# Kernel tuning notes

Hardware: AMD Instinct MI355X
Metric: run time of the kernel (lower is better)

Reference implementation:

```python
import jax, jax.numpy as jnp
import numpy as np

K = 7            # kernel size per spatial dim
HALF = K // 2    # 3
WIN = K * K      # 49


def _rel_dist():
    # matches torch: meshgrid('ij') of arange(k)-k//2, euclidean dist, flattened row-major
    c = np.arange(K, dtype=np.float32) - HALF
    gi, gj = np.meshgrid(c, c, indexing='ij')
    return jnp.asarray(np.sqrt(gi ** 2 + gj ** 2).reshape(-1))


def _unfold2d(t):
    B, H, W, C = t.shape
    p = jnp.pad(t, ((0, 0), (HALF, HALF), (HALF, HALF), (0, 0)))
    wins = [p[:, i:i + H, j:j + W, :] for i in range(K) for j in range(K)]
    return jnp.stack(wins, axis=3)


def setup_inputs() -> dict:
    key = jax.random.key(0)
    k1, k2, k3, k4, k5 = jax.random.split(key, 5)
    B, H, W, C = 4, 64, 64, 128
    x = jax.random.normal(k1, (B, H, W, C), dtype=jnp.float32)
    W_qkv = jax.random.normal(k2, (C, 3 * C), dtype=jnp.float32) * (C ** -0.5)
    # width_proj is zero-initialized in the module; use small random values to exercise the soft mask
    W_width = jax.random.normal(k3, (C, 1), dtype=jnp.float32) * 0.02
    b_width = jax.random.normal(k4, (1,), dtype=jnp.float32) * 0.02
    W_out = jax.random.normal(k5, (C, C), dtype=jnp.float32) * (C ** -0.5)
    return {"x": x, "W_qkv": W_qkv, "W_width": W_width, "b_width": b_width, "W_out": W_out}


def reference(x, W_qkv, W_width, b_width, W_out):
    B, H, W, C = x.shape
    L = H * W
    scale = C ** -0.5
    rel_dist = _rel_dist()
    max_dist = rel_dist.max()

    qkv = x @ W_qkv                              # (B,H,W,3C)
    q, k, v = jnp.split(qkv, 3, axis=-1)
    width = jax.nn.sigmoid(x @ W_width + b_width) * max_dist + 0.5  # (B,H,W,1)

    k_win = _unfold2d(k).reshape(B, L, WIN, C)
    v_win = _unfold2d(v).reshape(B, L, WIN, C)
    q_flat = q.reshape(B, L, C)
    width_flat = width.reshape(B, L, 1)

    scores = jnp.einsum('blc,blwc->blw', q_flat, k_win) * scale
    soft_mask = jax.nn.sigmoid((width_flat - rel_dist) * 5.0)
    scores = scores - (1.0 - soft_mask) * 10000.0
    attn = jax.nn.softmax(scores, axis=-1)
    out = jnp.einsum('blw,blwc->blc', attn, v_win).reshape(B, H, W, C)
    return (out + v) @ W_out
```

## Files before the change

kernel.cpp:

```cpp
#include <hip/hip_runtime.h>

#define C 128
#define NPIX 16384
#define THREE_C 384

typedef unsigned short u16;
typedef unsigned int u32;
typedef short bf16x8 __attribute__((ext_vector_type(8)));
typedef float f32x4 __attribute__((ext_vector_type(4)));

__device__ __forceinline__ float bf2f(u16 h) { return __uint_as_float(((u32)h) << 16); }
__device__ __forceinline__ u16 f2bf(float f) {
    u32 b = __float_as_uint(f);
    b += 0x7FFF + ((b >> 16) & 1);
    return (u16)(b >> 16);
}
__device__ __forceinline__ u32 pack2(float a, float b) {
    return (u32)f2bf(a) | ((u32)f2bf(b) << 16);
}

#define GST 136

__global__ __launch_bounds__(256) void qkv_kernel(const float* __restrict__ x,
                                                  const float* __restrict__ Wqkv,
                                                  const float* __restrict__ Wwidth,
                                                  const float* __restrict__ bwidth,
                                                  u16* __restrict__ qb,
                                                  u16* __restrict__ kb,
                                                  u16* __restrict__ vb,
                                                  float* __restrict__ width_g) {
    __shared__ u16 xs[64 * GST];
    __shared__ u16 wt[128 * GST];
    const int task = ((int)(blockIdx.x & 7)) * 96 + ((int)blockIdx.x >> 3);
    const int rb = task / 3;
    const int nb = task % 3;
    const int p0 = rb * 64;
    const int tid = threadIdx.x;
    const int wv = tid >> 6;
    const int l = tid & 63;
    const int l15 = l & 15;
    const int l4 = l >> 4;

#pragma unroll
    for (int t = 0; t < 8; ++t) {
        const int f = tid + t * 256;
        const int kq = f & 31, r = f >> 5;
        const float4 xv = *(const float4*)(x + (size_t)(p0 + r) * C + kq * 4);
        uint2 pk;
        pk.x = pack2(xv.x, xv.y);
        pk.y = pack2(xv.z, xv.w);
        *(uint2*)&xs[r * GST + kq * 4] = pk;
    }
#pragma unroll
    for (int t = 0; t < 16; ++t) {
        const int f = tid + t * 256;
        const int c = f & 127, kq = f >> 7;
        const float w0 = Wqkv[(size_t)(kq * 4 + 0) * THREE_C + nb * 128 + c];
        const float w1 = Wqkv[(size_t)(kq * 4 + 1) * THREE_C + nb * 128 + c];
        const float w2 = Wqkv[(size_t)(kq * 4 + 2) * THREE_C + nb * 128 + c];
        const float w3 = Wqkv[(size_t)(kq * 4 + 3) * THREE_C + nb * 128 + c];
        uint2 pk;
        pk.x = pack2(w0, w1);
        pk.y = pack2(w2, w3);
        *(uint2*)&wt[c * GST + kq * 4] = pk;
    }
    __syncthreads();

    if (nb == 0 && tid < 64) {
        float wacc = 0.f;
#pragma unroll
        for (int kk = 0; kk < C; ++kk) wacc += bf2f(xs[tid * GST + kk]) * Wwidth[kk];
        const float z = wacc + bwidth[0];
        width_g[p0 + tid] = (1.f / (1.f + __expf(-z))) * 4.242640687f + 0.5f;
    }

    const int strip = wv * 16;
    bf16x8 af[4];
#pragma unroll
    for (int kf = 0; kf < 4; ++kf)
        af[kf] = *(const bf16x8*)&xs[(strip + l15) * GST + kf * 32 + l4 * 8];

    f32x4 acc[8];
#pragma unroll
    for (int nf = 0; nf < 8; ++nf) acc[nf] = (f32x4){0.f, 0.f, 0.f, 0.f};
#pragma unroll
    for (int nf = 0; nf < 8; ++nf) {
#pragma unroll
        for (int kf = 0; kf < 4; ++kf) {
            const bf16x8 bf = *(const bf16x8*)&wt[(nf * 16 + l15) * GST + kf * 32 + l4 * 8];
            acc[nf] = __builtin_amdgcn_mfma_f32_16x16x32_bf16(af[kf], bf, acc[nf], 0, 0, 0);
        }
    }

    u16* dst = (nb == 0) ? qb : (nb == 1) ? kb : vb;
#pragma unroll
    for (int nf = 0; nf < 8; ++nf) {
        const int col = nf * 16 + l15;
#pragma unroll
        for (int r = 0; r < 4; ++r) {
            const int row = strip + l4 * 4 + r;
            dst[(size_t)(p0 + row) * C + col] = f2bf(acc[nf][r]);
        }
    }
}

#define HSTRIDE 136
#define TSTRIDE 232
#define VSWZ(ch, h) ((h) ^ ((((ch) >> 3) & 3) << 3))

__global__ __launch_bounds__(1024) void attn_kernel(const u16* __restrict__ qb,
                                                    const u16* __restrict__ kb,
                                                    const u16* __restrict__ vb,
                                                    const float* __restrict__ width_g,
                                                    const float* __restrict__ Wout,
                                                    float* __restrict__ out) {
    __shared__ u16 Kl[208 * HSTRIDE];
    __shared__ u16 Vt[128 * TSTRIDE];
    __shared__ u16 Pl[64 * TSTRIDE];
    __shared__ float rmax[4][64];
    __shared__ float rsum[4][64];
    __shared__ float wdl[64];

    const int tid = threadIdx.x;
    const int wv = tid >> 6;
    const int l = tid & 63;
    const int l15 = l & 15;
    const int l4 = l >> 4;

    const int W = ((int)blockIdx.x & 7) * 32 + ((int)blockIdx.x >> 3);
    const int b = W >> 6;
    const int t = W & 63;
    const int i0 = (t >> 3) * 8;
    const int j0 = (t & 7) * 8;
    const int pbase = b * 4096;

    if (tid < 64)
        wdl[tid] = width_g[pbase + (i0 + (tid >> 3)) * 64 + j0 + (tid & 7)];

#pragma unroll
    for (int u = 0; u < 5; ++u) {
        const int f = tid + u * 1024;
        if (f < 3328) {
            const int c = f & 15, h = f >> 4;
            uint4 val = make_uint4(0, 0, 0, 0);
            if (h < 196) {
                const int hi = (h * 2341) >> 15;
                const int hj = h - hi * 14;
                const int ii = i0 - 3 + hi, jj = j0 - 3 + hj;
                if (((unsigned)ii < 64u) && ((unsigned)jj < 64u))
                    val = *(const uint4*)(kb + (size_t)(pbase + ii * 64 + jj) * C + c * 8);
            }
            *(uint4*)&Kl[h * HSTRIDE + c * 8] = val;
        } else {
            const int f2 = f - 3328;
            const int c8 = f2 & 15, h = (f2 >> 4) * 2;
            union { uint4 u4; u16 us[8]; } va, vz;
            va.u4 = make_uint4(0, 0, 0, 0);
            vz.u4 = make_uint4(0, 0, 0, 0);
            {
                const int hi = (h * 2341) >> 15;
                const int hj = h - hi * 14;
                const int ii = i0 - 3 + hi, jj = j0 - 3 + hj;
                if ((h < 196) && ((unsigned)ii < 64u) && ((unsigned)jj < 64u))
                    va.u4 = *(const uint4*)(vb + (size_t)(pbase + ii * 64 + jj) * C + c8 * 8);
            }
            {
                const int h1 = h + 1;
                const int hi = (h1 * 2341) >> 15;
                const int hj = h1 - hi * 14;
                const int ii = i0 - 3 + hi, jj = j0 - 3 + hj;
                if ((h1 < 196) && ((unsigned)ii < 64u) && ((unsigned)jj < 64u))
                    vz.u4 = *(const uint4*)(vb + (size_t)(pbase + ii * 64 + jj) * C + c8 * 8);
            }
#pragma unroll
            for (int s = 0; s < 8; ++s) {
                const int ch = c8 * 8 + s;
                *(u32*)&Vt[ch * TSTRIDE + VSWZ(ch, h)] = (u32)va.us[s] | ((u32)vz.us[s] << 16);
            }
        }
    }

    const int strip = wv >> 2;
    const int g = wv & 3;
    bf16x8 qf[4];
    {
        const int qr = strip * 16 + l15;
        const int p = pbase + (i0 + (qr >> 3)) * 64 + j0 + (qr & 7);
#pragma unroll
        for (int kf = 0; kf < 4; ++kf)
            qf[kf] = *(const bf16x8*)(qb + (size_t)p * C + kf * 32 + l4 * 8);
    }
    __syncthreads();

    f32x4 sv[4];
#pragma unroll
    for (int tt = 0; tt < 4; ++tt) {
        const int nf = g + 4 * tt;
        f32x4 acc = {0.f, 0.f, 0.f, 0.f};
        if (nf < 13) {
            const u16* kr = Kl + (nf * 16 + l15) * HSTRIDE + l4 * 8;
#pragma unroll
            for (int kf = 0; kf < 4; ++kf)
                acc = __builtin_amdgcn_mfma_f32_16x16x32_bf16(
                    qf[kf], *(const bf16x8*)(kr + kf * 32), acc, 0, 0, 0);
        }
        sv[tt] = acc;
    }

    const int qrb = strip * 16 + l4 * 4;
    float wdr[4], mxr[4];
#pragma unroll
    for (int r = 0; r < 4; ++r) { wdr[r] = wdl[qrb + r]; mxr[r] = -3.0e38f; }
#pragma unroll
    for (int tt = 0; tt < 4; ++tt) {
        const int nf = g + 4 * tt;
        if (nf < 13) {
            const int n = nf * 16 + l15;
            const int hi = (n * 2341) >> 15;
            const int hj = n - hi * 14;
#pragma unroll
            for (int r = 0; r < 4; ++r) {
                const int qr = qrb + r;
                const int di = hi - 3 - (qr >> 3);
                const int dj = hj - 3 - (qr & 7);
                const bool valid = ((unsigned)(di + 3) <= 6u) && ((unsigned)(dj + 3) <= 6u);
                float s = -3.0e38f;
                if (valid) {
                    const float rd = sqrtf((float)(di * di + dj * dj));
                    const float sm = 1.f / (1.f + __expf(-5.f * (wdr[r] - rd)));
                    s = sv[tt][r] * 0.08838834765f - (1.f - sm) * 10000.f;
                }
                sv[tt][r] = s;
                mxr[r] = fmaxf(mxr[r], s);
            }
        } else {
#pragma unroll
            for (int r = 0; r < 4; ++r) sv[tt][r] = -3.0e38f;
        }
    }
#pragma unroll
    for (int r = 0; r < 4; ++r) {
        float m = mxr[r];
        m = fmaxf(m, __shfl_xor(m, 1));
        m = fmaxf(m, __shfl_xor(m, 2));
        m = fmaxf(m, __shfl_xor(m, 4));
        m = fmaxf(m, __shfl_xor(m, 8));
        mxr[r] = m;
    }
    float smr[4] = {0.f, 0.f, 0.f, 0.f};
#pragma unroll
    for (int tt = 0; tt < 4; ++tt) {
#pragma unroll
        for (int r = 0; r < 4; ++r) {
            const float e = __expf(sv[tt][r] - mxr[r]);
            sv[tt][r] = e;
            smr[r] += e;
        }
    }
#pragma unroll
    for (int r = 0; r < 4; ++r) {
        float s = smr[r];
        s += __shfl_xor(s, 1);
        s += __shfl_xor(s, 2);
        s += __shfl_xor(s, 4);
        s += __shfl_xor(s, 8);
        smr[r] = s;
    }
    if (l15 == 0) {
#pragma unroll
        for (int r = 0; r < 4; ++r) {
            rmax[g][qrb + r] = mxr[r];
            rsum[g][qrb + r] = smr[r];
        }
    }
    __syncthreads();

    u16* wtl = Kl;
#pragma unroll
    for (int tq = 0; tq < 4; ++tq) {
        const int f = tid + tq * 1024;
        const int c = f & 127, kq = f >> 7;
        const float w0 = Wout[(size_t)(kq * 4 + 0) * C + c];
        const float w1 = Wout[(size_t)(kq * 4 + 1) * C + c];
        const float w2 = Wout[(size_t)(kq * 4 + 2) * C + c];
        const float w3 = Wout[(size_t)(kq * 4 + 3) * C + c];
        uint2 pk;
        pk.x = pack2(w0, w1);
        pk.y = pack2(w2, w3);
        *(uint2*)&wtl[c * GST + kq * 4] = pk;
    }

    float fac[4];
#pragma unroll
    for (int r = 0; r < 4; ++r) {
        const int qr = qrb + r;
        const float m0 = rmax[0][qr], m1 = rmax[1][qr], m2 = rmax[2][qr], m3 = rmax[3][qr];
        const float mf = fmaxf(fmaxf(m0, m1), fmaxf(m2, m3));
        const float tot = rsum[0][qr] * __expf(m0 - mf) + rsum[1][qr] * __expf(m1 - mf)
                        + rsum[2][qr] * __expf(m2 - mf) + rsum[3][qr] * __expf(m3 - mf);
        fac[r] = __expf(mxr[r] - mf) / tot;
    }
#pragma unroll
    for (int tt = 0; tt < 4; ++tt) {
        const int nf = g + 4 * tt;
        if (nf < 13) {
            const int n = nf * 16 + l15;
#pragma unroll
            for (int r = 0; r < 4; ++r)
                Pl[(qrb + r) * TSTRIDE + n] = f2bf(sv[tt][r] * fac[r]);
        } else if (nf == 13) {
            const int n = 208 + l15;
#pragma unroll
            for (int r = 0; r < 4; ++r)
                Pl[(qrb + r) * TSTRIDE + n] = 0;
        }
    }
    __syncthreads();

    f32x4 oacc[2];
    oacc[0] = (f32x4){0.f, 0.f, 0.f, 0.f};
    oacc[1] = (f32x4){0.f, 0.f, 0.f, 0.f};
#pragma unroll
    for (int kf = 0; kf < 7; ++kf) {
        const bf16x8 pa = *(const bf16x8*)(Pl + (strip * 16 + l15) * TSTRIDE + kf * 32 + l4 * 8);
#pragma unroll
        for (int nf2 = 0; nf2 < 2; ++nf2) {
            const int ch = g * 32 + nf2 * 16 + l15;
            const bf16x8 vf = *(const bf16x8*)(Vt + ch * TSTRIDE + VSWZ(ch, kf * 32 + l4 * 8));
            oacc[nf2] = __builtin_amdgcn_mfma_f32_16x16x32_bf16(pa, vf, oacc[nf2], 0, 0, 0);
        }
    }

    u16* ylds = Kl + 128 * GST;
#pragma unroll
    for (int nf2 = 0; nf2 < 2; ++nf2) {
        const int cch = g * 32 + nf2 * 16 + l15;
#pragma unroll
        for (int r = 0; r < 4; ++r) {
            const int qr = qrb + r;
            const int h = 45 + (qr >> 3) * 14 + (qr & 7);
            const float vv = bf2f(Vt[cch * TSTRIDE + VSWZ(cch, h)]);
            ylds[qr * GST + cch] = f2bf(oacc[nf2][r] + vv);
        }
    }
    __syncthreads();

    bf16x8 yf[4];
#pragma unroll
    for (int kf = 0; kf < 4; ++kf)
        yf[kf] = *(const bf16x8*)&ylds[(strip * 16 + l15) * GST + kf * 32 + l4 * 8];

    f32x4 oc[2];
    oc[0] = (f32x4){0.f, 0.f, 0.f, 0.f};
    oc[1] = (f32x4){0.f, 0.f, 0.f, 0.f};
#pragma unroll
    for (int u = 0; u < 2; ++u) {
        const int nf = g + 4 * u;
#pragma unroll
        for (int kf = 0; kf < 4; ++kf) {
            const bf16x8 bf = *(const bf16x8*)&wtl[(nf * 16 + l15) * GST + kf * 32 + l4 * 8];
            oc[u] = __builtin_amdgcn_mfma_f32_16x16x32_bf16(yf[kf], bf, oc[u], 0, 0, 0);
        }
    }
#pragma unroll
    for (int u = 0; u < 2; ++u) {
        const int col = (g + 4 * u) * 16 + l15;
#pragma unroll
        for (int r = 0; r < 4; ++r) {
            const int qr = qrb + r;
            const int p = pbase + (i0 + (qr >> 3)) * 64 + j0 + (qr & 7);
            out[(size_t)p * C + col] = oc[u][r];
        }
    }
}

extern "C" void kernel_launch(void* const* d_in, const int* in_sizes, int n_in,
                              void* d_out, int out_size, void* d_ws, size_t ws_size,
                              hipStream_t stream) {
    const float* x      = (const float*)d_in[0];
    const float* Wqkv   = (const float*)d_in[1];
    const float* Wwidth = (const float*)d_in[2];
    const float* bwidth = (const float*)d_in[3];
    const float* Wout   = (const float*)d_in[4];
    float* out = (float*)d_out;

    u16* qb = (u16*)d_ws;
    u16* kb = qb + (size_t)NPIX * C;
    u16* vb = kb + (size_t)NPIX * C;
    float* width = (float*)(vb + (size_t)NPIX * C);

    qkv_kernel<<<768, 256, 0, stream>>>(x, Wqkv, Wwidth, bwidth, qb, kb, vb, width);
    attn_kernel<<<256, 1024, 0, stream>>>(qb, kb, vb, width, Wout, out);
}
```

Before: 30.01 us.

## Pretranspose Wout to bf16 in qkv kernel and batch K/V halo loads

The first kernel now converts W_out once into a transposed bf16 buffer in the workspace. The attention kernel prefetches that buffer into registers early and writes it to LDS later, replacing 256 blocks each doing strided fp32 loads and packing. The K/V halo gather is restructured so all global loads are issued before any LDS stores, which raises memory-level parallelism at the cost of more registers. The Vt row stride is also padded slightly to change the LDS bank mapping.

```diff
diff --git a/kernel.cpp b/kernel.cpp
--- a/kernel.cpp
+++ b/kernel.cpp
@@ -25,10 +25,12 @@
                                                   const float* __restrict__ Wqkv,
                                                   const float* __restrict__ Wwidth,
                                                   const float* __restrict__ bwidth,
+                                                  const float* __restrict__ Wout,
                                                   u16* __restrict__ qb,
                                                   u16* __restrict__ kb,
                                                   u16* __restrict__ vb,
-                                                  float* __restrict__ width_g) {
+                                                  float* __restrict__ width_g,
+                                                  u16* __restrict__ wot) {
     __shared__ u16 xs[64 * GST];
     __shared__ u16 wt[128 * GST];
     const int task = ((int)(blockIdx.x & 7)) * 96 + ((int)blockIdx.x >> 3);
@@ -64,6 +66,16 @@
         pk.y = pack2(w2, w3);
         *(uint2*)&wt[c * GST + kq * 4] = pk;
     }
+    if (task < 8) {
+        const int base = (task * 256 + tid) * 8;
+        const int c = base >> 7, k0 = base & 127;
+        uint4 pk;
+        pk.x = pack2(Wout[(size_t)(k0 + 0) * C + c], Wout[(size_t)(k0 + 1) * C + c]);
+        pk.y = pack2(Wout[(size_t)(k0 + 2) * C + c], Wout[(size_t)(k0 + 3) * C + c]);
+        pk.z = pack2(Wout[(size_t)(k0 + 4) * C + c], Wout[(size_t)(k0 + 5) * C + c]);
+        pk.w = pack2(Wout[(size_t)(k0 + 6) * C + c], Wout[(size_t)(k0 + 7) * C + c]);
+        *(uint4*)&wot[base] = pk;
+    }
     __syncthreads();
 
     if (nb == 0 && tid < 64) {
@@ -105,14 +117,14 @@
 }
 
 #define HSTRIDE 136
-#define TSTRIDE 232
+#define TSTRIDE 236
 #define VSWZ(ch, h) ((h) ^ ((((ch) >> 3) & 3) << 3))
 
 __global__ __launch_bounds__(1024) void attn_kernel(const u16* __restrict__ qb,
                                                     const u16* __restrict__ kb,
                                                     const u16* __restrict__ vb,
                                                     const float* __restrict__ width_g,
-                                                    const float* __restrict__ Wout,
+                                                    const u16* __restrict__ wot,
                                                     float* __restrict__ out) {
     __shared__ u16 Kl[208 * HSTRIDE];
     __shared__ u16 Vt[128 * TSTRIDE];
@@ -137,32 +149,42 @@
     if (tid < 64)
         wdl[tid] = width_g[pbase + (i0 + (tid >> 3)) * 64 + j0 + (tid & 7)];
 
-#pragma unroll
-    for (int u = 0; u < 5; ++u) {
-        const int f = tid + u * 1024;
-        if (f < 3328) {
-            const int c = f & 15, h = f >> 4;
-            uint4 val = make_uint4(0, 0, 0, 0);
-            if (h < 196) {
-                const int hi = (h * 2341) >> 15;
-                const int hj = h - hi * 14;
-                const int ii = i0 - 3 + hi, jj = j0 - 3 + hj;
-                if (((unsigned)ii < 64u) && ((unsigned)jj < 64u))
-                    val = *(const uint4*)(kb + (size_t)(pbase + ii * 64 + jj) * C + c * 8);
-            }
-            *(uint4*)&Kl[h * HSTRIDE + c * 8] = val;
-        } else {
-            const int f2 = f - 3328;
-            const int c8 = f2 & 15, h = (f2 >> 4) * 2;
-            union { uint4 u4; u16 us[8]; } va, vz;
-            va.u4 = make_uint4(0, 0, 0, 0);
-            vz.u4 = make_uint4(0, 0, 0, 0);
+    const uint4 z4 = make_uint4(0, 0, 0, 0);
+    uint4 kreg[4];
+    int koff[4];
+    bool kw[4];
+#pragma unroll
+    for (int rr = 0; rr < 4; ++rr) {
+        const int f = tid + rr * 1024;
+        kw[rr] = (f < 3328);
+        kreg[rr] = z4;
+        const int c = f & 15, h = f >> 4;
+        koff[rr] = h * HSTRIDE + c * 8;
+        if (kw[rr] && h < 196) {
+            const int hi = (h * 2341) >> 15;
+            const int hj = h - hi * 14;
+            const int ii = i0 - 3 + hi, jj = j0 - 3 + hj;
+            if (((unsigned)ii < 64u) && ((unsigned)jj < 64u))
+                kreg[rr] = *(const uint4*)(kb + (size_t)(pbase + ii * 64 + jj) * C + c * 8);
+        }
+    }
+    uint4 va[2], vz[2];
+    int vc8[2], vh[2];
+    bool vw[2];
+#pragma unroll
+    for (int rr = 0; rr < 2; ++rr) {
+        const int f = tid + rr * 1024;
+        vw[rr] = (f < 1792);
+        va[rr] = z4; vz[rr] = z4;
+        const int c8 = f & 15, h = ((f >> 4) * 2) & 255;
+        vc8[rr] = c8; vh[rr] = h;
+        if (vw[rr]) {
             {
                 const int hi = (h * 2341) >> 15;
                 const int hj = h - hi * 14;
                 const int ii = i0 - 3 + hi, jj = j0 - 3 + hj;
                 if ((h < 196) && ((unsigned)ii < 64u) && ((unsigned)jj < 64u))
-                    va.u4 = *(const uint4*)(vb + (size_t)(pbase + ii * 64 + jj) * C + c8 * 8);
+                    va[rr] = *(const uint4*)(vb + (size_t)(pbase + ii * 64 + jj) * C + c8 * 8);
             }
             {
                 const int h1 = h + 1;
@@ -170,12 +192,23 @@
                 const int hj = h1 - hi * 14;
                 const int ii = i0 - 3 + hi, jj = j0 - 3 + hj;
                 if ((h1 < 196) && ((unsigned)ii < 64u) && ((unsigned)jj < 64u))
-                    vz.u4 = *(const uint4*)(vb + (size_t)(pbase + ii * 64 + jj) * C + c8 * 8);
+                    vz[rr] = *(const uint4*)(vb + (size_t)(pbase + ii * 64 + jj) * C + c8 * 8);
             }
+        }
+    }
+#pragma unroll
+    for (int rr = 0; rr < 4; ++rr)
+        if (kw[rr]) *(uint4*)&Kl[koff[rr]] = kreg[rr];
+#pragma unroll
+    for (int rr = 0; rr < 2; ++rr) {
+        if (vw[rr]) {
+            union { uint4 u4; u16 us[8]; } ua, uz;
+            ua.u4 = va[rr]; uz.u4 = vz[rr];
+            const int c8 = vc8[rr], h = vh[rr];
 #pragma unroll
             for (int s = 0; s < 8; ++s) {
                 const int ch = c8 * 8 + s;
-                *(u32*)&Vt[ch * TSTRIDE + VSWZ(ch, h)] = (u32)va.us[s] | ((u32)vz.us[s] << 16);
+                *(u32*)&Vt[ch * TSTRIDE + VSWZ(ch, h)] = (u32)ua.us[s] | ((u32)uz.us[s] << 16);
             }
         }
     }
@@ -206,6 +239,9 @@
         }
         sv[tt] = acc;
     }
+
+    uint4 wcopy0 = *(const uint4*)(wot + tid * 8);
+    uint4 wcopy1 = *(const uint4*)(wot + (tid + 1024) * 8);
 
     const int qrb = strip * 16 + l4 * 4;
     float wdr[4], mxr[4];
@@ -276,18 +312,11 @@
     __syncthreads();
 
     u16* wtl = Kl;
-#pragma unroll
-    for (int tq = 0; tq < 4; ++tq) {
-        const int f = tid + tq * 1024;
-        const int c = f & 127, kq = f >> 7;
-        const float w0 = Wout[(size_t)(kq * 4 + 0) * C + c];
-        const float w1 = Wout[(size_t)(kq * 4 + 1) * C + c];
-        const float w2 = Wout[(size_t)(kq * 4 + 2) * C + c];
-        const float w3 = Wout[(size_t)(kq * 4 + 3) * C + c];
-        uint2 pk;
-        pk.x = pack2(w0, w1);
-        pk.y = pack2(w2, w3);
-        *(uint2*)&wtl[c * GST + kq * 4] = pk;
+    {
+        const int c0 = tid >> 4, k0 = (tid & 15) * 8;
+        *(uint4*)&wtl[c0 * GST + k0] = wcopy0;
+        const int c1 = 64 + (tid >> 4);
+        *(uint4*)&wtl[c1 * GST + k0] = wcopy1;
     }
 
     float fac[4];
@@ -388,7 +417,8 @@
     u16* kb = qb + (size_t)NPIX * C;
     u16* vb = kb + (size_t)NPIX * C;
     float* width = (float*)(vb + (size_t)NPIX * C);
-
-    qkv_kernel<<<768, 256, 0, stream>>>(x, Wqkv, Wwidth, bwidth, qb, kb, vb, width);
-    attn_kernel<<<256, 1024, 0, stream>>>(qb, kb, vb, width, Wout, out);
+    u16* wot = (u16*)(width + NPIX);
+
+    qkv_kernel<<<768, 256, 0, stream>>>(x, Wqkv, Wwidth, bwidth, Wout, qb, kb, vb, width, wot);
+    attn_kernel<<<256, 1024, 0, stream>>>(qb, kb, vb, width, wot, out);
 }
```

After: 29.57 us. Within noise of the previous version (-1.5%).
